# Optimization experiments

Hardware: AMD Instinct MI355X
Metric: run time of the kernel (lower is better)

The kernel has to match this reference:

```python
import jax, jax.numpy as jnp
import numpy as np

RES = (512, 512)
MAX_VAL = 100.0
OBJ_WIDTH = 5
N_ITERS = 5
SIGMA = 0.2


def setup_inputs() -> dict:
    key = jax.random.key(0)
    ks = jax.random.split(key, 6)
    H, W = RES
    x = jax.random.uniform(ks[0], (1, H, W, 2), jnp.float32) * 2.0 - 1.0  # query grid in [-1,1]
    boundary_types = jax.random.randint(ks[1], (H, W), 0, 2, jnp.int32)
    boundary_conditions = jax.random.uniform(ks[2], (H, W), jnp.float32)
    B_enc = SIGMA * jax.random.normal(ks[3], (64, 2), jnp.float32)  # GaussianEncoding(0.2, 2, 64)
    Wh = jax.random.normal(ks[4], (4, 128, 128), jnp.float32) / jnp.sqrt(128.0)
    W_out = jax.random.normal(ks[5], (128, 1), jnp.float32) / jnp.sqrt(128.0)
    return {"x": x, "boundary_types": boundary_types,
            "boundary_conditions": boundary_conditions,
            "B_enc": B_enc, "Wh": Wh, "W_out": W_out}


def _box_filter(a, width):
    # width x width mean filter, 'same' padding (F.conv2d with ones/width^2 kernel)
    k = jnp.ones((1, 1, width, width), a.dtype) / float(width * width)
    return jax.lax.conv_general_dilated(a[None, None], k, (1, 1), "SAME")[0, 0]


def _grid_sample_2d(img, grid):
    # img [H,W]; grid [N,2] with (x,y) in [-1,1]; bilinear, align_corners=True, border padding
    H, W = img.shape
    ix = jnp.clip((grid[:, 0] + 1.0) * 0.5 * (W - 1), 0.0, W - 1.0)
    iy = jnp.clip((grid[:, 1] + 1.0) * 0.5 * (H - 1), 0.0, H - 1.0)
    x0 = jnp.floor(ix).astype(jnp.int32)
    y0 = jnp.floor(iy).astype(jnp.int32)
    x1 = jnp.clip(x0 + 1, 0, W - 1)
    y1 = jnp.clip(y0 + 1, 0, H - 1)
    wx = ix - x0
    wy = iy - y0
    return (img[y0, x0] * (1 - wx) * (1 - wy) + img[y0, x1] * wx * (1 - wy)
            + img[y1, x0] * (1 - wx) * wy + img[y1, x1] * wx * wy)


def _solve(V0, C, boundary_types, boundary_conditions):
    # 5 Jacobi-style 8-neighbor stencil passes: free cells take the neighbor
    # average plus local cost; boundary cells are pinned to their conditions.
    free = boundary_types == 0

    def step(V, _):
        Vp = jnp.pad(V, 1, mode="edge")
        nb = (Vp[:-2, :-2] + Vp[:-2, 1:-1] + Vp[:-2, 2:]
              + Vp[1:-1, :-2] + Vp[1:-1, 2:]
              + Vp[2:, :-2] + Vp[2:, 1:-1] + Vp[2:, 2:]) / 8.0
        return jnp.where(free, nb + C, boundary_conditions), None

    V, _ = jax.lax.scan(step, V0, None, length=N_ITERS)
    return V


def reference(x, boundary_types, boundary_conditions, B_enc, Wh, W_out):
    H, W = RES
    free = boundary_types == 0
    # V init: max_val everywhere, boundary cells pinned (obj_inds = boundary_types > 0)
    V0 = jnp.where(free, jnp.float32(MAX_VAL), boundary_conditions)

    # Gaussian random Fourier feature encoding of 0.5 + 0.5*x -> 128 dims
    xq = 0.5 + 0.5 * x.reshape(-1, 2)
    vp = (2.0 * jnp.pi) * (xq @ B_enc.T)            # [N, 64]
    enc = jnp.concatenate([jnp.cos(vp), jnp.sin(vp)], axis=-1)  # [N, 128]

    # FullyFusedMLP: 4 hidden ReLU layers of 128 neurons, linear 1-dim output, no bias
    h = enc
    for i in range(Wh.shape[0]):
        h = jax.nn.relu(h @ Wh[i])
    C = (h @ W_out).reshape(H, W)
    C_pos = jax.nn.relu(C)

    # extra cost: box-filtered obstacle boundary values splashed onto free cells
    obj = boundary_conditions * (boundary_types == 1) * (boundary_conditions > 0)
    extra = _box_filter(obj, OBJ_WIDTH) * free
    Cs = C_pos + extra

    out_grid = _solve(V0, Cs, boundary_types, boundary_conditions)
    out = _grid_sample_2d(out_grid, x.reshape(-1, 2)).reshape(H, W)
    return out, C
```

## Files before the change

kernel.cpp:

```cpp
#include <hip/hip_runtime.h>
#include <hip/hip_bf16.h>


typedef unsigned short ushort_t;
typedef short short8 __attribute__((ext_vector_type(8)));
typedef float floatx16 __attribute__((ext_vector_type(16)));
typedef unsigned int uintx4 __attribute__((ext_vector_type(4)));

#define HH 512
#define WW 512
#define NPIX (HH*WW)

__device__ inline unsigned int pk_bf16(float a, float b) {
    __hip_bfloat162 h = __float22bfloat162_rn(float2{a, b});
    return *(unsigned int*)&h;
}
__device__ inline void async_copy16(void* lds, const void* g) {
    __builtin_amdgcn_global_load_lds(
        (const __attribute__((address_space(1))) unsigned int*)g,
        (__attribute__((address_space(3))) unsigned int*)lds, 16, 0, 0);
}

__global__ __launch_bounds__(256) void prep_kernel(const float* __restrict__ Wh,
                                                   ushort_t* __restrict__ WT) {
    __shared__ float trans[32][129];
    const int t = threadIdx.x;
    const int l = blockIdx.x >> 2, n0 = (blockIdx.x & 3) * 32;
    const int nl = t & 31, k0 = t >> 5;
    #pragma unroll
    for (int pass = 0; pass < 16; ++pass) {
        int k = pass * 8 + k0;
        trans[nl][k] = Wh[l * 16384 + k * 128 + n0 + nl];
    }
    __syncthreads();
    #pragma unroll
    for (int c = 0; c < 2; ++c) {
        int idx = c * 256 + t;
        int nl2 = idx >> 4, P = idx & 15;
        int n = n0 + nl2;
        int cc = P ^ (n & 15);
        int kk = cc * 8;
        unsigned int w0 = pk_bf16(trans[nl2][kk + 0], trans[nl2][kk + 1]);
        unsigned int w1 = pk_bf16(trans[nl2][kk + 2], trans[nl2][kk + 3]);
        unsigned int w2 = pk_bf16(trans[nl2][kk + 4], trans[nl2][kk + 5]);
        unsigned int w3 = pk_bf16(trans[nl2][kk + 6], trans[nl2][kk + 7]);
        ((uint4*)WT)[(l * 128 + n) * 16 + P] = uint4{w0, w1, w2, w3};
    }
}

__global__ __launch_bounds__(512, 2) void mlp_kernel(const float* __restrict__ x,
                                                     const ushort_t* __restrict__ WT,
                                                     const float* __restrict__ benc,
                                                     const float* __restrict__ wout,
                                                     float* __restrict__ C_ws,
                                                     float* __restrict__ outbuf) {
    __shared__ __align__(16) ushort_t wlds[128 * 128];
    const int tid = threadIdx.x;
    const int lane = tid & 63, wave = tid >> 6;
    const int m = lane & 31, Hh = lane >> 5;
    const int p0 = blockIdx.x * 256 + wave * 32;

    #pragma unroll
    for (int c2 = 0; c2 < 4; ++c2) {
        int base = c2 * 512 + wave * 64;
        async_copy16(&wlds[base * 8], (const char*)WT + (base + lane) * 16);
    }

    uintx4 fragv[8];

    {
        float2 xv = ((const float2*)x)[p0 + m];
        float xq0 = 0.5f + 0.5f * xv.x, xq1 = 0.5f + 0.5f * xv.y;
        #pragma unroll
        for (int ks = 0; ks < 4; ++ks) {
            #pragma unroll
            for (int jp = 0; jp < 4; ++jp) {
                int f = ks * 16 + Hh * 8 + jp * 2;
                float4 b = *(const float4*)&benc[2 * f];
                float t0 = __builtin_amdgcn_fractf(xq0 * b.x + xq1 * b.y);
                float t1 = __builtin_amdgcn_fractf(xq0 * b.z + xq1 * b.w);
                fragv[ks][jp]     = pk_bf16(__builtin_amdgcn_cosf(t0),
                                            __builtin_amdgcn_cosf(t1));
                fragv[ks + 4][jp] = pk_bf16(__builtin_amdgcn_sinf(t0),
                                            __builtin_amdgcn_sinf(t1));
            }
        }
    }
    __syncthreads();

    floatx16 acc[4];
    #pragma unroll 1
    for (int l = 0; l < 4; ++l) {
        #pragma unroll
        for (int i = 0; i < 4; ++i) acc[i] = (floatx16)(0.0f);

        #pragma unroll
        for (int ks = 0; ks < 8; ++ks) {
            short8 bf = __builtin_bit_cast(short8, fragv[ks]);
            #pragma unroll
            for (int i = 0; i < 4; ++i) {
                int n = i * 32 + m;
                int cc = 2 * ks + Hh;
                short8 av = *(const short8*)&wlds[(n << 7) + ((cc ^ (n & 15)) << 3)];
                acc[i] = __builtin_amdgcn_mfma_f32_32x32x16_bf16(av, bf, acc[i], 0, 0, 0);
            }
        }
        if (l == 3) break;

        __syncthreads();

        #pragma unroll
        for (int c2 = 0; c2 < 4; ++c2) {
            int base = c2 * 512 + wave * 64;
            async_copy16(&wlds[base * 8],
                         (const char*)WT + (l + 1) * 32768 + (base + lane) * 16);
        }

        #pragma unroll
        for (int ks = 0; ks < 8; ++ks) {
            const int i = ks >> 1, par = ks & 1;
            unsigned int u0 = pk_bf16(fmaxf(acc[i][8 * par + 0], 0.0f),
                                      fmaxf(acc[i][8 * par + 1], 0.0f));
            unsigned int u1 = pk_bf16(fmaxf(acc[i][8 * par + 2], 0.0f),
                                      fmaxf(acc[i][8 * par + 3], 0.0f));
            unsigned int u2 = pk_bf16(fmaxf(acc[i][8 * par + 4], 0.0f),
                                      fmaxf(acc[i][8 * par + 5], 0.0f));
            unsigned int u3 = pk_bf16(fmaxf(acc[i][8 * par + 6], 0.0f),
                                      fmaxf(acc[i][8 * par + 7], 0.0f));
            unsigned int s0 = Hh ? u0 : u2, s1 = Hh ? u1 : u3;
            unsigned int k0 = Hh ? u2 : u0, k1 = Hh ? u3 : u1;
            unsigned int r0 = (unsigned int)__shfl_xor((int)s0, 32);
            unsigned int r1 = (unsigned int)__shfl_xor((int)s1, 32);
            fragv[ks][0] = Hh ? r0 : k0;
            fragv[ks][1] = Hh ? r1 : k1;
            fragv[ks][2] = Hh ? k0 : r0;
            fragv[ks][3] = Hh ? k1 : r1;
        }

        __syncthreads();
    }

    float s = 0.0f;
    #pragma unroll
    for (int i = 0; i < 4; ++i) {
        #pragma unroll
        for (int rq = 0; rq < 4; ++rq) {
            float4 wv = *(const float4*)&wout[i * 32 + rq * 8 + 4 * Hh];
            s += fmaxf(acc[i][rq * 4 + 0], 0.0f) * wv.x
               + fmaxf(acc[i][rq * 4 + 1], 0.0f) * wv.y
               + fmaxf(acc[i][rq * 4 + 2], 0.0f) * wv.z
               + fmaxf(acc[i][rq * 4 + 3], 0.0f) * wv.w;
        }
    }
    s += __shfl_xor(s, 32);
    if (Hh == 0) {
        C_ws[p0 + m] = s;
        outbuf[NPIX + p0 + m] = s;
    }
}

__global__ __launch_bounds__(256) void fused_solve_kernel(const int* __restrict__ bt,
                                                          const float* __restrict__ bc,
                                                          const float* __restrict__ C_ws,
                                                          float* __restrict__ Vfin) {
    __shared__ float Va[30 * 32];
    __shared__ float Vb[30 * 32];
    __shared__ float Wp[30 * 32];
    const int tid = threadIdx.x;
    const int gx0 = (blockIdx.x & 31) * 16 - 7, gy0 = (blockIdx.x >> 5) * 16 - 7;

    for (int c = tid; c < 30 * 32; c += 256) {
        int li = c >> 5, lj = c & 31;
        int gi = gy0 + li, gj = gx0 + lj;
        float v = 0.0f;
        if (lj < 30 && gi >= 0 && gi < HH && gj >= 0 && gj < WW) {
            int g = gi * WW + gj;
            float b = bc[g];
            if (bt[g] == 1 && b > 0.0f) v = b;
        }
        Va[c] = v;
    }
    __syncthreads();

    for (int c = tid; c < 30 * 32; c += 256) {
        int li = c >> 5, lj = c & 31;
        int gi = gy0 + li, gj = gx0 + lj;
        float w = -1.0f, v0 = 0.0f;
        if (li >= 2 && li < 28 && lj >= 2 && lj < 28 &&
            gi >= 0 && gi < HH && gj >= 0 && gj < WW) {
            int g = gi * WW + gj;
            if (bt[g] == 0) {
                float s = 0.0f;
                #pragma unroll
                for (int di = 0; di < 5; ++di)
                    #pragma unroll
                    for (int dj = 0; dj < 5; ++dj)
                        s += Va[(li + di - 2) * 32 + lj + dj - 2];
                w = fmaxf(C_ws[g], 0.0f) + s * 0.04f;
                v0 = 100.0f;
            } else {
                float b = bc[g];
                w = -b - 1.0f;
                v0 = b;
            }
        }
        Wp[c] = w;
        Vb[c] = v0;
    }
    __syncthreads();

    float* src = Vb;
    float* dst = Va;
    #pragma unroll 1
    for (int t = 0; t < 5; ++t) {
        for (int c = tid; c < 26 * 32; c += 256) {
            int li = 2 + (c >> 5), lj = c & 31;
            if (lj < 2 || lj >= 28) continue;
            float w = Wp[li * 32 + lj];
            float v;
            if (w < 0.0f) {
                v = -w - 1.0f;
            } else {
                int gi = gy0 + li, gj = gx0 + lj;
                int um = (gi > 0)      ? li - 1 : li;
                int dp = (gi < HH - 1) ? li + 1 : li;
                int lm = (gj > 0)      ? lj - 1 : lj;
                int rp = (gj < WW - 1) ? lj + 1 : lj;
                float s = src[um * 32 + lm] + src[um * 32 + lj] + src[um * 32 + rp]
                        + src[li * 32 + lm]                     + src[li * 32 + rp]
                        + src[dp * 32 + lm] + src[dp * 32 + lj] + src[dp * 32 + rp];
                v = s * 0.125f + w;
            }
            dst[li * 32 + lj] = v;
        }
        __syncthreads();
        float* tmp = src; src = dst; dst = tmp;
    }

    {
        int li = 7 + (tid >> 4), lj = 7 + (tid & 15);
        Vfin[(gy0 + li) * WW + gx0 + lj] = src[li * 32 + lj];
    }
}

__global__ void sample_kernel(const float* __restrict__ x,
                              const float* __restrict__ V,
                              float* __restrict__ out) {
    int idx = blockIdx.x * 256 + threadIdx.x;
    float2 g2 = ((const float2*)x)[idx];
    float ix = (g2.x + 1.0f) * 0.5f * 511.0f;
    float iy = (g2.y + 1.0f) * 0.5f * 511.0f;
    ix = fminf(fmaxf(ix, 0.0f), 511.0f);
    iy = fminf(fmaxf(iy, 0.0f), 511.0f);
    int x0 = (int)floorf(ix), y0 = (int)floorf(iy);
    int x1 = min(x0 + 1, 511), y1 = min(y0 + 1, 511);
    float wx = ix - (float)x0, wy = iy - (float)y0;
    float v00 = V[y0 * 512 + x0], v01 = V[y0 * 512 + x1];
    float v10 = V[y1 * 512 + x0], v11 = V[y1 * 512 + x1];
    float v = v00 * (1.0f - wx) * (1.0f - wy) + v01 * wx * (1.0f - wy)
            + v10 * (1.0f - wx) * wy          + v11 * wx * wy;
    out[idx] = v;
}

extern "C" void kernel_launch(void* const* d_in, const int* in_sizes, int n_in,
                              void* d_out, int out_size, void* d_ws, size_t ws_size,
                              hipStream_t stream) {
    const float* x    = (const float*)d_in[0];
    const int*   bt   = (const int*)d_in[1];
    const float* bc   = (const float*)d_in[2];
    const float* benc = (const float*)d_in[3];
    const float* Wh   = (const float*)d_in[4];
    const float* wout = (const float*)d_in[5];

    char* ws = (char*)d_ws;
    ushort_t* WT   = (ushort_t*)(ws + 4096);
    float*    C_ws = (float*)(ws + 262144);
    float*    Vfin = (float*)(ws + 262144 + 3 * (1 << 20));
    float*    outp = (float*)d_out;

    prep_kernel<<<16, 256, 0, stream>>>(Wh, WT);
    mlp_kernel<<<1024, 512, 0, stream>>>(x, WT, benc, wout, C_ws, outp);
    fused_solve_kernel<<<1024, 256, 0, stream>>>(bt, bc, C_ws, Vfin);
    sample_kernel<<<1024, 256, 0, stream>>>(x, Vfin, outp);
}
```

Before: 122.0 us.

## Permute hidden-feature K order so MFMA outputs feed next layer without shuffles

Reorders the K dimension of the packed bf16 weight matrices and the Fourier-encoding fragments so that the accumulator layout of one MFMA layer directly matches the B-operand layout of the next. This removes the per-layer cross-half-wave shuffle exchange (two shfl_xor per k-step plus selects) between hidden layers. The weight prep and encoding index maps become more intricate, and correctness depends on the permutation being applied consistently to weights and activations.

Result: no change. 120.2 us (-1.4%).

```diff
diff --git a/kernel.cpp b/kernel.cpp
--- a/kernel.cpp
+++ b/kernel.cpp
@@ -39,11 +39,12 @@
         int nl2 = idx >> 4, P = idx & 15;
         int n = n0 + nl2;
         int cc = P ^ (n & 15);
-        int kk = cc * 8;
-        unsigned int w0 = pk_bf16(trans[nl2][kk + 0], trans[nl2][kk + 1]);
-        unsigned int w1 = pk_bf16(trans[nl2][kk + 2], trans[nl2][kk + 3]);
-        unsigned int w2 = pk_bf16(trans[nl2][kk + 4], trans[nl2][kk + 5]);
-        unsigned int w3 = pk_bf16(trans[nl2][kk + 6], trans[nl2][kk + 7]);
+        int ks = cc >> 1, Hq = cc & 1;
+        int base = (ks >> 1) * 32 + (ks & 1) * 16 + Hq * 4;
+        unsigned int w0 = pk_bf16(trans[nl2][base + 0],  trans[nl2][base + 1]);
+        unsigned int w1 = pk_bf16(trans[nl2][base + 2],  trans[nl2][base + 3]);
+        unsigned int w2 = pk_bf16(trans[nl2][base + 8],  trans[nl2][base + 9]);
+        unsigned int w3 = pk_bf16(trans[nl2][base + 10], trans[nl2][base + 11]);
         ((uint4*)WT)[(l * 128 + n) * 16 + P] = uint4{w0, w1, w2, w3};
     }
 }
@@ -72,17 +73,19 @@
         float2 xv = ((const float2*)x)[p0 + m];
         float xq0 = 0.5f + 0.5f * xv.x, xq1 = 0.5f + 0.5f * xv.y;
         #pragma unroll
-        for (int ks = 0; ks < 4; ++ks) {
+        for (int ks = 0; ks < 8; ++ks) {
+            const int i = ks >> 1, par = ks & 1;
             #pragma unroll
             for (int jp = 0; jp < 4; ++jp) {
-                int f = ks * 16 + Hh * 8 + jp * 2;
+                int nu = i * 32 + par * 16 + Hh * 4 + (jp & 1) * 2 + (jp >> 1) * 8;
+                int f = nu & 63;
                 float4 b = *(const float4*)&benc[2 * f];
                 float t0 = __builtin_amdgcn_fractf(xq0 * b.x + xq1 * b.y);
                 float t1 = __builtin_amdgcn_fractf(xq0 * b.z + xq1 * b.w);
-                fragv[ks][jp]     = pk_bf16(__builtin_amdgcn_cosf(t0),
-                                            __builtin_amdgcn_cosf(t1));
-                fragv[ks + 4][jp] = pk_bf16(__builtin_amdgcn_sinf(t0),
-                                            __builtin_amdgcn_sinf(t1));
+                float v0, v1;
+                if (ks < 4) { v0 = __builtin_amdgcn_cosf(t0); v1 = __builtin_amdgcn_cosf(t1); }
+                else        { v0 = __builtin_amdgcn_sinf(t0); v1 = __builtin_amdgcn_sinf(t1); }
+                fragv[ks][jp] = pk_bf16(v0, v1);
             }
         }
     }
@@ -119,22 +122,14 @@
         #pragma unroll
         for (int ks = 0; ks < 8; ++ks) {
             const int i = ks >> 1, par = ks & 1;
-            unsigned int u0 = pk_bf16(fmaxf(acc[i][8 * par + 0], 0.0f),
-                                      fmaxf(acc[i][8 * par + 1], 0.0f));
-            unsigned int u1 = pk_bf16(fmaxf(acc[i][8 * par + 2], 0.0f),
-                                      fmaxf(acc[i][8 * par + 3], 0.0f));
-            unsigned int u2 = pk_bf16(fmaxf(acc[i][8 * par + 4], 0.0f),
-                                      fmaxf(acc[i][8 * par + 5], 0.0f));
-            unsigned int u3 = pk_bf16(fmaxf(acc[i][8 * par + 6], 0.0f),
-                                      fmaxf(acc[i][8 * par + 7], 0.0f));
-            unsigned int s0 = Hh ? u0 : u2, s1 = Hh ? u1 : u3;
-            unsigned int k0 = Hh ? u2 : u0, k1 = Hh ? u3 : u1;
-            unsigned int r0 = (unsigned int)__shfl_xor((int)s0, 32);
-            unsigned int r1 = (unsigned int)__shfl_xor((int)s1, 32);
-            fragv[ks][0] = Hh ? r0 : k0;
-            fragv[ks][1] = Hh ? r1 : k1;
-            fragv[ks][2] = Hh ? k0 : r0;
-            fragv[ks][3] = Hh ? k1 : r1;
+            fragv[ks][0] = pk_bf16(fmaxf(acc[i][8 * par + 0], 0.0f),
+                                   fmaxf(acc[i][8 * par + 1], 0.0f));
+            fragv[ks][1] = pk_bf16(fmaxf(acc[i][8 * par + 2], 0.0f),
+                                   fmaxf(acc[i][8 * par + 3], 0.0f));
+            fragv[ks][2] = pk_bf16(fmaxf(acc[i][8 * par + 4], 0.0f),
+                                   fmaxf(acc[i][8 * par + 5], 0.0f));
+            fragv[ks][3] = pk_bf16(fmaxf(acc[i][8 * par + 6], 0.0f),
+                                   fmaxf(acc[i][8 * par + 7], 0.0f));
         }
 
         __syncthreads();
```
